# Optimization experiments

Hardware: AMD Instinct MI355X
Metric: run time of the kernel (lower is better)

The kernel has to match this reference:

```python
import jax, jax.numpy as jnp
import numpy as np

D_MODEL = 1024
NUM_HEADS = 16
HEAD_DIM = D_MODEL // NUM_HEADS
FFN_HIDDEN = 4096
EPS = 1e-5


def setup_inputs() -> dict:
    key = jax.random.key(0)
    ks = jax.random.split(key, 7)
    s = 0.02
    return {
        "x": jax.random.normal(ks[0], (2, 2048, D_MODEL), dtype=jnp.float32),
        "W_qkv": jax.random.normal(ks[1], (D_MODEL, 3 * D_MODEL), dtype=jnp.float32) * s,
        "b_qkv": jnp.zeros((3 * D_MODEL,), dtype=jnp.float32),
        "W_o": jax.random.normal(ks[2], (D_MODEL, D_MODEL), dtype=jnp.float32) * s,
        "b_o": jnp.zeros((D_MODEL,), dtype=jnp.float32),
        "gamma1": jnp.ones((D_MODEL,), dtype=jnp.float32),
        "beta1": jnp.zeros((D_MODEL,), dtype=jnp.float32),
        "W1": jax.random.normal(ks[3], (D_MODEL, FFN_HIDDEN), dtype=jnp.float32) * s,
        "b1": jnp.zeros((FFN_HIDDEN,), dtype=jnp.float32),
        "W2": jax.random.normal(ks[4], (FFN_HIDDEN, D_MODEL), dtype=jnp.float32) * s,
        "b2": jnp.zeros((D_MODEL,), dtype=jnp.float32),
        "gamma2": jnp.ones((D_MODEL,), dtype=jnp.float32),
        "beta2": jnp.zeros((D_MODEL,), dtype=jnp.float32),
    }


def _layernorm(x, gamma, beta):
    mean = jnp.mean(x, axis=-1, keepdims=True)
    var = jnp.mean((x - mean) ** 2, axis=-1, keepdims=True)
    return gamma * (x - mean) / jnp.sqrt(var + EPS) + beta


def reference(x, W_qkv, b_qkv, W_o, b_o, gamma1, beta1, W1, b1, W2, b2, gamma2, beta2):
    B, S, D = x.shape
    # ---- multi-head attention ----
    qkv = x @ W_qkv + b_qkv                       # [B,S,3D]
    qkv = qkv.reshape(B, S, NUM_HEADS, 3 * HEAD_DIM).transpose(0, 2, 1, 3)  # [B,H,S,3hd]
    q, k, v = jnp.split(qkv, 3, axis=-1)          # each [B,H,S,hd]
    scores = jnp.einsum("bhqd,bhkd->bhqk", q, k) / np.sqrt(HEAD_DIM)
    attn = jax.nn.softmax(scores, axis=-1)
    vals = jnp.einsum("bhqk,bhkd->bhqd", attn, v)
    vals = vals.transpose(0, 2, 1, 3).reshape(B, S, D)
    attn_out = vals @ W_o + b_o
    # dropout disabled (eval mode)
    h = _layernorm(attn_out + x, gamma1, beta1)
    # ---- position-wise FFN (dropout before relu per source, disabled) ----
    ffn = jax.nn.relu(h @ W1 + b1) @ W2 + b2
    return _layernorm(ffn + h, gamma2, beta2)
```

## Files before the change

### kernel.cpp

```cpp
#include <hip/hip_runtime.h>
#include <stdint.h>

typedef float v4f __attribute__((ext_vector_type(4)));
typedef __bf16 v8bf __attribute__((ext_vector_type(8)));
typedef __bf16 v4bf __attribute__((ext_vector_type(4)));
typedef unsigned short v8us __attribute__((ext_vector_type(8)));
typedef unsigned short v4us __attribute__((ext_vector_type(4)));

__device__ __forceinline__ float b2f(unsigned short u) {
    union { float f; uint32_t i; } x; x.i = ((uint32_t)u) << 16; return x.f;
}
__device__ __forceinline__ unsigned short f2b(float f) {
    union { float f; uint32_t u; } x; x.f = f;
    uint32_t r = x.u + 0x7fffu + ((x.u >> 16) & 1u);
    return (unsigned short)(r >> 16);
}

__device__ __forceinline__ void gload16(const unsigned short* g, unsigned short* l) {
    __builtin_amdgcn_global_load_lds(
        (const __attribute__((address_space(1))) void*)g,
        (__attribute__((address_space(3))) void*)l,
        16, 0, 0);
}

__device__ __forceinline__ void transpose_tile(
    const float* __restrict__ W, unsigned short* __restrict__ WT,
    int K, int N, int kb, int nb, int tid)
{
    __shared__ unsigned short t[64][65];
    const int r = tid >> 4, c4 = (tid & 15) * 4;
    #pragma unroll
    for (int i = 0; i < 4; ++i) {
        int k = r + i * 16;
        float4 v = *(const float4*)&W[(size_t)(kb + k) * N + nb + c4];
        t[c4 + 0][k] = f2b(v.x);
        t[c4 + 1][k] = f2b(v.y);
        t[c4 + 2][k] = f2b(v.z);
        t[c4 + 3][k] = f2b(v.w);
    }
    __syncthreads();
    #pragma unroll
    for (int i = 0; i < 4; ++i) {
        int n = r + i * 16;
        v4us o = {t[n][c4], t[n][c4 + 1], t[n][c4 + 2], t[n][c4 + 3]};
        *(v4us*)&WT[(size_t)(nb + n) * K + kb + c4] = o;
    }
}

__global__ __launch_bounds__(256) void prep_fused(
    const float* __restrict__ x, unsigned short* __restrict__ xb,
    const float* __restrict__ Wqkv, unsigned short* __restrict__ WqkvT,
    const float* __restrict__ W1, unsigned short* __restrict__ W1T,
    const float* __restrict__ Wo, unsigned short* __restrict__ WoT)
{
    const int b = blockIdx.x, tid = threadIdx.x;
    if (b < 4096) {
        int i = (b * 256 + tid) * 4;
        float4 v = *(const float4*)&x[i];
        v4us o = {f2b(v.x), f2b(v.y), f2b(v.z), f2b(v.w)};
        *(v4us*)&xb[i] = o;
    } else if (b < 4096 + 768) {
        int lb = b - 4096;
        transpose_tile(Wqkv, WqkvT, 1024, 3072, (lb / 48) * 64, (lb % 48) * 64, tid);
    } else if (b < 4096 + 768 + 1024) {
        int lb = b - 4096 - 768;
        transpose_tile(W1, W1T, 1024, 4096, (lb / 64) * 64, (lb % 64) * 64, tid);
    } else {
        int lb = b - 4096 - 768 - 1024;
        transpose_tile(Wo, WoT, 1024, 1024, (lb / 16) * 64, (lb % 16) * 64, tid);
    }
}

__global__ __launch_bounds__(256) void transpose_to_bt(
    const float* __restrict__ W, unsigned short* __restrict__ WT, int K, int N)
{
    transpose_tile(W, WT, K, N, blockIdx.y * 64, blockIdx.x * 64, threadIdx.x);
}

__device__ __forceinline__ void xcd_swizzle(int& bm, int& bn) {
    int NB = gridDim.x, MB = gridDim.y;
    int flat = blockIdx.x + NB * blockIdx.y;
    int xcd = flat & 7, j = flat >> 3;
    int MBand = MB >> 3;
    bm = xcd * MBand + (j % MBand);
    bn = j / MBand;
}

__global__ __launch_bounds__(256) void gemm_bt_n64(
    const unsigned short* __restrict__ A, const unsigned short* __restrict__ BT,
    const float* __restrict__ bias, unsigned short* __restrict__ C,
    int M, int N, int K, int relu)
{
    __shared__ __align__(16) unsigned short sA0[2][128 * 32];
    __shared__ __align__(16) unsigned short sB0[2][64 * 32];
    __shared__ __align__(16) unsigned short sA1[2][128 * 32];
    __shared__ __align__(16) unsigned short sB1[2][64 * 32];
    const int tid  = threadIdx.x;
    const int wave = tid >> 6, lane = tid & 63;
    const int wm = wave >> 1, wn = wave & 1;
    const int quad = lane >> 4, l16 = lane & 15;
    int bm, bn;
    xcd_swizzle(bm, bn);

    const int srow = lane >> 2, scol = (lane & 3) * 8;
    const unsigned short* ga0 = A  + (size_t)(bm * 128 + (wave * 2 + 0) * 16 + srow) * K + scol;
    const unsigned short* ga1 = A  + (size_t)(bm * 128 + (wave * 2 + 1) * 16 + srow) * K + scol;
    const unsigned short* gb0 = BT + (size_t)(bn * 64 + wave * 16 + srow) * K + scol;
    const int oa0 = (wave * 2 + 0) * 512 + lane * 8;
    const int oa1 = (wave * 2 + 1) * 512 + lane * 8;
    const int ob  = wave * 512 + lane * 8;

    v8us aR0[2][2], bR0[2], aR1[2][2], bR1[2];
    #pragma unroll
    for (int c = 0; c < 2; ++c) {
        aR0[c][0] = *(const v8us*)(ga0 + c * 32);
        aR0[c][1] = *(const v8us*)(ga1 + c * 32);
        bR0[c]    = *(const v8us*)(gb0 + c * 32);
        aR1[c][0] = *(const v8us*)(ga0 + 64 + c * 32);
        aR1[c][1] = *(const v8us*)(ga1 + 64 + c * 32);
        bR1[c]    = *(const v8us*)(gb0 + 64 + c * 32);
    }

    v4f acc[4][2];
    #pragma unroll
    for (int i = 0; i < 4; ++i)
        #pragma unroll
        for (int j = 0; j < 2; ++j)
            acc[i][j] = (v4f){0.f, 0.f, 0.f, 0.f};

    for (int kt = 0; kt < K; kt += 128) {
        #pragma unroll
        for (int c = 0; c < 2; ++c) {
            *(v8us*)&sA0[c][oa0] = aR0[c][0];
            *(v8us*)&sA0[c][oa1] = aR0[c][1];
            *(v8us*)&sB0[c][ob]  = bR0[c];
        }
        __syncthreads();
        if (kt + 128 < K) {
            const int kn = kt + 128;
            #pragma unroll
            for (int c = 0; c < 2; ++c) {
                aR0[c][0] = *(const v8us*)(ga0 + kn + c * 32);
                aR0[c][1] = *(const v8us*)(ga1 + kn + c * 32);
                bR0[c]    = *(const v8us*)(gb0 + kn + c * 32);
            }
        }
        #pragma unroll
        for (int c = 0; c < 2; ++c) {
            v8bf af[4], bfr[2];
            #pragma unroll
            for (int mt = 0; mt < 4; ++mt)
                af[mt] = *(const v8bf*)&sA0[c][(wm * 64 + mt * 16 + l16) * 32 + quad * 8];
            #pragma unroll
            for (int nt = 0; nt < 2; ++nt)
                bfr[nt] = *(const v8bf*)&sB0[c][(wn * 32 + nt * 16 + l16) * 32 + quad * 8];
            #pragma unroll
            for (int mt = 0; mt < 4; ++mt)
                #pragma unroll
                for (int nt = 0; nt < 2; ++nt)
                    acc[mt][nt] = __builtin_amdgcn_mfma_f32_16x16x32_bf16(
                        af[mt], bfr[nt], acc[mt][nt], 0, 0, 0);
        }

        #pragma unroll
        for (int c = 0; c < 2; ++c) {
            *(v8us*)&sA1[c][oa0] = aR1[c][0];
            *(v8us*)&sA1[c][oa1] = aR1[c][1];
            *(v8us*)&sB1[c][ob]  = bR1[c];
        }
        __syncthreads();
        if (kt + 192 < K) {
            const int kn = kt + 192;
            #pragma unroll
            for (int c = 0; c < 2; ++c) {
                aR1[c][0] = *(const v8us*)(ga0 + kn + c * 32);
                aR1[c][1] = *(const v8us*)(ga1 + kn + c * 32);
                bR1[c]    = *(const v8us*)(gb0 + kn + c * 32);
            }
        }
        #pragma unroll
        for (int c = 0; c < 2; ++c) {
            v8bf af[4], bfr[2];
            #pragma unroll
            for (int mt = 0; mt < 4; ++mt)
                af[mt] = *(const v8bf*)&sA1[c][(wm * 64 + mt * 16 + l16) * 32 + quad * 8];
            #pragma unroll
            for (int nt = 0; nt < 2; ++nt)
                bfr[nt] = *(const v8bf*)&sB1[c][(wn * 32 + nt * 16 + l16) * 32 + quad * 8];
            #pragma unroll
            for (int mt = 0; mt < 4; ++mt)
                #pragma unroll
                for (int nt = 0; nt < 2; ++nt)
                    acc[mt][nt] = __builtin_amdgcn_mfma_f32_16x16x32_bf16(
                        af[mt], bfr[nt], acc[mt][nt], 0, 0, 0);
        }
    }

    #pragma unroll
    for (int mt = 0; mt < 4; ++mt) {
        #pragma unroll
        for (int nt = 0; nt < 2; ++nt) {
            int col = bn * 64 + wn * 32 + nt * 16 + l16;
            float bv = bias ? bias[col] : 0.f;
            #pragma unroll
            for (int r = 0; r < 4; ++r) {
                int row = bm * 128 + wm * 64 + mt * 16 + quad * 4 + r;
                float v = acc[mt][nt][r] + bv;
                if (relu) v = fmaxf(v, 0.f);
                C[(size_t)row * N + col] = f2b(v);
            }
        }
    }
}

template<int SPLIT_V>
__global__ __launch_bounds__(512) void gemm256(
    const unsigned short* __restrict__ A, const unsigned short* __restrict__ BT,
    const float* __restrict__ bias, unsigned short* __restrict__ C,
    unsigned short* __restrict__ VT, int M, int N, int K, int relu)
{
    __shared__ __align__(16) unsigned short sA[2][256 * 64];
    __shared__ __align__(16) unsigned short sB[2][256 * 64];
    const int tid  = threadIdx.x;
    const int wave = tid >> 6, lane = tid & 63;
    const int wm = wave >> 2, wn = wave & 3;
    const int quad = lane >> 4, l16 = lane & 15;
    int bm, bn;
    xcd_swizzle(bm, bn);

    const int srow = lane >> 3;
    const int scol = ((lane & 7) * 8) ^ ((lane & 32) ? 16 : 0);
    size_t aoff[4], boff[4];
    #pragma unroll
    for (int j = 0; j < 4; ++j) {
        int r = wave * 32 + j * 8 + srow;
        aoff[j] = (size_t)(bm * 256 + r) * K + scol;
        boff[j] = (size_t)(bn * 256 + r) * K + scol;
    }
    const int lds0 = wave * 32 * 64;

    const int ksw = (quad * 8) ^ ((l16 & 4) ? 16 : 0);

    v4f acc[8][4];
    #pragma unroll
    for (int i = 0; i < 8; ++i)
        #pragma unroll
        for (int j = 0; j < 4; ++j)
            acc[i][j] = (v4f){0.f, 0.f, 0.f, 0.f};

    const int NT = K >> 6;
    #pragma unroll
    for (int j = 0; j < 4; ++j) {
        gload16(A  + aoff[j], &sA[0][lds0 + j * 512]);
        gload16(BT + boff[j], &sB[0][lds0 + j * 512]);
    }
    __syncthreads();

    for (int t = 0; t < NT; ++t) {
        const int buf = t & 1;
        if (t + 1 < NT) {
            const int ktn = (t + 1) << 6;
            #pragma unroll
            for (int j = 0; j < 4; ++j) {
                gload16(A  + aoff[j] + ktn, &sA[buf ^ 1][lds0 + j * 512]);
                gload16(BT + boff[j] + ktn, &sB[buf ^ 1][lds0 + j * 512]);
            }
        }

        v8bf bfr[4][2];
        #pragma unroll
        for (int nt2 = 0; nt2 < 4; ++nt2)
            #pragma unroll
            for (int kc = 0; kc < 2; ++kc)
                bfr[nt2][kc] = *(const v8bf*)&sB[buf][
                    (wn * 64 + nt2 * 16 + l16) * 64 + kc * 32 + ksw];
        #pragma unroll
        for (int mq = 0; mq < 2; ++mq) {
            v8bf af[4][2];
            #pragma unroll
            for (int mt2 = 0; mt2 < 4; ++mt2)
                #pragma unroll
                for (int kc = 0; kc < 2; ++kc)
                    af[mt2][kc] = *(const v8bf*)&sA[buf][
                        (wm * 128 + mq * 64 + mt2 * 16 + l16) * 64 + kc * 32 + ksw];
            #pragma unroll
            for (int mt2 = 0; mt2 < 4; ++mt2)
                #pragma unroll
                for (int nt2 = 0; nt2 < 4; ++nt2)
                    #pragma unroll
                    for (int kc = 0; kc < 2; ++kc)
                        acc[mq * 4 + mt2][nt2] =
                            __builtin_amdgcn_mfma_f32_16x16x32_bf16(
                                af[mt2][kc], bfr[nt2][kc],
                                acc[mq * 4 + mt2][nt2], 0, 0, 0);
        }
        __syncthreads();
    }

    #pragma unroll
    for (int mt = 0; mt < 8; ++mt) {
        int row = bm * 256 + wm * 128 + mt * 16 + quad * 4;
        #pragma unroll
        for (int nt = 0; nt < 4; ++nt) {
            int c0 = bn * 256 + wn * 64 + nt * 16;
            int col = c0 + l16;
            float bv = bias ? bias[col] : 0.f;
            if (SPLIT_V && (c0 % 192) >= 128) {
                int hh = c0 / 192;
                int d  = (c0 % 192) - 128 + l16;
                int bb = row >> 11;
                int s  = row & 2047;
                v4us st;
                #pragma unroll
                for (int r = 0; r < 4; ++r)
                    st[r] = f2b(acc[mt][nt][r] + bv);
                *(v4us*)&VT[((size_t)(bb * 16 + hh) * 64 + d) * 2048 + s] = st;
            } else {
                float qs = (SPLIT_V && (c0 % 192) < 64) ? 0.18033688f : 1.0f;
                #pragma unroll
                for (int r = 0; r < 4; ++r) {
                    float v = (acc[mt][nt][r] + bv) * qs;
                    if (relu) v = fmaxf(v, 0.f);
                    C[(size_t)(row + r) * N + col] = f2b(v);
                }
            }
        }
    }
}

__global__ __launch_bounds__(512) void attn_mfma(
    const unsigned short* __restrict__ qkv, const unsigned short* __restrict__ VT,
    unsigned short* __restrict__ av)
{
    __shared__ __align__(16) unsigned short sK[2][64 * 72];
    __shared__ __align__(16) unsigned short sVT[2][64 * 72];
    __shared__ __align__(16) unsigned short sP[8][16 * 72];
    const int tid  = threadIdx.x;
    const int wave = tid >> 6, lane = tid & 63;
    const int quad = lane >> 4, l16 = lane & 15;
    const int blk = blockIdx.x;
    const int xcd = blk & 7, local = blk >> 3;
    const int bh = xcd * 4 + (local & 3);
    const int qb = local >> 2;
    const int h = bh & 15, b = bh >> 4;
    const int row0 = b * 2048;
    const int qbase = row0 + qb * 128 + wave * 16;
    const size_t qoff = (size_t)h * 192;
    const size_t koff = qoff + 64;

    v8bf qf[2];
    #pragma unroll
    for (int kc = 0; kc < 2; ++kc)
        qf[kc] = *(const v8bf*)&qkv[(size_t)(qbase + l16) * 3072
                                    + qoff + kc * 32 + quad * 8];

    v4f o[4];
    #pragma unroll
    for (int dt = 0; dt < 4; ++dt)
        o[dt] = (v4f){0.f, 0.f, 0.f, 0.f};
    float ll = 0.f;

    const int k_key = tid >> 3, k_oct = (tid & 7) * 8;
    const unsigned short* gK = qkv + (size_t)(row0 + k_key) * 3072 + koff + k_oct;
    const unsigned short* gV = VT + ((size_t)bh * 64 + k_key) * 2048 + k_oct;
    const size_t stepK = (size_t)64 * 3072;
    const size_t stepV = 64;

    v8us kreg = *(const v8us*)gK;
    v8us vreg = *(const v8us*)gV;
    gK += stepK; gV += stepV;

    for (int kt = 0; kt < 32; ++kt) {
        const int cur = kt & 1;
        *(v8us*)&sK[cur][k_key * 72 + k_oct]  = kreg;
        *(v8us*)&sVT[cur][k_key * 72 + k_oct] = vreg;
        __syncthreads();
        if (kt < 31) {
            kreg = *(const v8us*)gK;
            vreg = *(const v8us*)gV;
            gK += stepK; gV += stepV;
        }

        v4f sc[4];
        #pragma unroll
        for (int kk = 0; kk < 4; ++kk) {
            sc[kk] = (v4f){0.f, 0.f, 0.f, 0.f};
            #pragma unroll
            for (int kc = 0; kc < 2; ++kc) {
                v8bf ak = *(const v8bf*)&sK[cur][(kk * 16 + l16) * 72 + kc * 32 + quad * 8];
                sc[kk] = __builtin_amdgcn_mfma_f32_16x16x32_bf16(
                    ak, qf[kc], sc[kk], 0, 0, 0);
            }
        }

        float ps = 0.f;
        #pragma unroll
        for (int kk = 0; kk < 4; ++kk) {
            v4bf pk;
            #pragma unroll
            for (int rr = 0; rr < 4; ++rr) {
                float p = __builtin_amdgcn_exp2f(sc[kk][rr]);
                ps += p;
                pk[rr] = (__bf16)p;
            }
            *(v4bf*)&sP[wave][l16 * 72 + kk * 16 + quad * 4] = pk;
        }
        ll += ps;

        __asm__ volatile("s_waitcnt lgkmcnt(0)" ::: "memory");

        #pragma unroll
        for (int c = 0; c < 2; ++c) {
            union { v8bf v; v8us u; } u;
            u.u = *(const v8us*)&sP[wave][l16 * 72 + c * 32 + quad * 8];
            v8bf pb = u.v;
            #pragma unroll
            for (int dt = 0; dt < 4; ++dt) {
                v8bf va = *(const v8bf*)&sVT[cur][(dt * 16 + l16) * 72 + c * 32 + quad * 8];
                o[dt] = __builtin_amdgcn_mfma_f32_16x16x32_bf16(
                    va, pb, o[dt], 0, 0, 0);
            }
        }
    }

    float l = ll;
    l += __shfl_xor(l, 16, 64);
    l += __shfl_xor(l, 32, 64);
    float inv = 1.f / l;
    int qrow = qbase + l16;
    #pragma unroll
    for (int dt = 0; dt < 4; ++dt) {
        v4bf st;
        #pragma unroll
        for (int rr = 0; rr < 4; ++rr)
            st[rr] = (__bf16)(o[dt][rr] * inv);
        *(v4bf*)&av[(size_t)qrow * 1024 + h * 64 + dt * 16 + quad * 4] = st;
    }
}

template<int RES_F32, int OUT_F32>
__global__ __launch_bounds__(256) void ln_fused(
    const unsigned short* __restrict__ a, const void* __restrict__ residv,
    const float* __restrict__ gamma, const float* __restrict__ beta,
    void* __restrict__ outv)
{
    const int row = blockIdx.x, tid = threadIdx.x;
    const size_t base = (size_t)row * 1024;
    const int c0 = tid * 4;
    ushort4 avv = *(const ushort4*)&a[base + c0];
    float y[4];
    if (RES_F32) {
        float4 rv = *(const float4*)((const float*)residv + base + c0);
        y[0] = b2f(avv.x) + rv.x;
        y[1] = b2f(avv.y) + rv.y;
        y[2] = b2f(avv.z) + rv.z;
        y[3] = b2f(avv.w) + rv.w;
    } else {
        ushort4 rv = *(const ushort4*)((const unsigned short*)residv + base + c0);
        y[0] = b2f(avv.x) + b2f(rv.x);
        y[1] = b2f(avv.y) + b2f(rv.y);
        y[2] = b2f(avv.z) + b2f(rv.z);
        y[3] = b2f(avv.w) + b2f(rv.w);
    }
    float s  = y[0] + y[1] + y[2] + y[3];
    float ss = y[0]*y[0] + y[1]*y[1] + y[2]*y[2] + y[3]*y[3];
    #pragma unroll
    for (int off = 32; off; off >>= 1) {
        s  += __shfl_xor(s, off, 64);
        ss += __shfl_xor(ss, off, 64);
    }
    __shared__ float red[8];
    int wave = tid >> 6, lane = tid & 63;
    if (lane == 0) { red[wave] = s; red[4 + wave] = ss; }
    __syncthreads();
    s  = red[0] + red[1] + red[2] + red[3];
    ss = red[4] + red[5] + red[6] + red[7];
    float mean = s * (1.f / 1024.f);
    float var  = ss * (1.f / 1024.f) - mean * mean;
    float rstd = rsqrtf(var + 1e-5f);
    float4 gv = *(const float4*)&gamma[c0];
    float4 bv = *(const float4*)&beta[c0];
    float r0 = gv.x * (y[0] - mean) * rstd + bv.x;
    float r1 = gv.y * (y[1] - mean) * rstd + bv.y;
    float r2 = gv.z * (y[2] - mean) * rstd + bv.z;
    float r3 = gv.w * (y[3] - mean) * rstd + bv.w;
    if (OUT_F32) {
        float4 ov = {r0, r1, r2, r3};
        *(float4*)((float*)outv + base + c0) = ov;
    } else {
        ushort4 ov;
        ov.x = f2b(r0); ov.y = f2b(r1); ov.z = f2b(r2); ov.w = f2b(r3);
        *(ushort4*)((unsigned short*)outv + base + c0) = ov;
    }
}

extern "C" void kernel_launch(void* const* d_in, const int* in_sizes, int n_in,
                              void* d_out, int out_size, void* d_ws, size_t ws_size,
                              hipStream_t stream)
{
    (void)in_sizes; (void)n_in; (void)out_size; (void)ws_size;
    const float* x    = (const float*)d_in[0];
    const float* Wqkv = (const float*)d_in[1];
    const float* bqkv = (const float*)d_in[2];
    const float* Wo   = (const float*)d_in[3];
    const float* bo   = (const float*)d_in[4];
    const float* g1   = (const float*)d_in[5];
    const float* be1  = (const float*)d_in[6];
    const float* W1   = (const float*)d_in[7];
    const float* b1   = (const float*)d_in[8];
    const float* W2   = (const float*)d_in[9];
    const float* b2   = (const float*)d_in[10];
    const float* g2   = (const float*)d_in[11];
    const float* be2  = (const float*)d_in[12];
    float* out = (float*)d_out;

    unsigned short* R0 = (unsigned short*)d_ws;
    unsigned short* R1 = R0 + (size_t)16 * 1024 * 1024;
    unsigned short* R2 = R1 + (size_t)4 * 1024 * 1024;
    unsigned short* R3 = R2 + (size_t)4 * 1024 * 1024;
    unsigned short* WqkvT = R0 + (size_t)12 * 1024 * 1024;
    unsigned short* WoT   = R0 + (size_t)15 * 1024 * 1024;

    const int M = 4096;
    dim3 blk(256);

    prep_fused<<<dim3(4096 + 768 + 1024 + 256), blk, 0, stream>>>(
        x, R2, Wqkv, WqkvT, W1, R3, Wo, WoT);
    gemm256<1><<<dim3(12, 16), dim3(512), 0, stream>>>(R2, WqkvT, bqkv, R0, R1, M, 3072, 1024, 0);
    attn_mfma<<<dim3(512), dim3(512), 0, stream>>>(R0, R1, R2);
    gemm_bt_n64<<<dim3(16, 32), blk, 0, stream>>>(R2, WoT, bo, R1, M, 1024, 1024, 0);
    ln_fused<1, 0><<<dim3(4096), blk, 0, stream>>>(R1, x, g1, be1, R1);
    transpose_to_bt<<<dim3(16, 64), blk, 0, stream>>>(W2, R2, 4096, 1024);
    gemm256<0><<<dim3(16, 16), dim3(512), 0, stream>>>(R1, R3, b1, R0, nullptr, M, 4096, 1024, 1);
    gemm_bt_n64<<<dim3(16, 32), blk, 0, stream>>>(R0, R2, b2, R3, M, 1024, 4096, 0);
    ln_fused<0, 1><<<dim3(4096), blk, 0, stream>>>(R3, R1, g2, be2, out);
}
```

Baseline: 337.2 us.

## Switch gemm256 to triple-buffered K=32 tiles with explicit waitcnt pipelining

Changes the 256x256 GEMM mainloop from double-buffered 64-wide K tiles to triple-buffered 32-wide K tiles. Global-to-LDS loads are issued two stages ahead and gated with explicit vmcnt waits and raw barriers instead of __syncthreads. MFMA issue priority is raised with s_setprio. The XOR swizzle on LDS reads is dropped, which risks more bank conflicts, and the smaller K step doubles the number of barriers per K.

New measurement: 360.2 us. 1.07x slower.

```diff
diff --git a/kernel.cpp b/kernel.cpp
--- a/kernel.cpp
+++ b/kernel.cpp
@@ -219,8 +219,8 @@
     const float* __restrict__ bias, unsigned short* __restrict__ C,
     unsigned short* __restrict__ VT, int M, int N, int K, int relu)
 {
-    __shared__ __align__(16) unsigned short sA[2][256 * 64];
-    __shared__ __align__(16) unsigned short sB[2][256 * 64];
+    __shared__ __align__(16) unsigned short sA[3][256 * 32];
+    __shared__ __align__(16) unsigned short sB[3][256 * 32];
     const int tid  = threadIdx.x;
     const int wave = tid >> 6, lane = tid & 63;
     const int wm = wave >> 2, wn = wave & 3;
@@ -228,18 +228,15 @@
     int bm, bn;
     xcd_swizzle(bm, bn);
 
-    const int srow = lane >> 3;
-    const int scol = ((lane & 7) * 8) ^ ((lane & 32) ? 16 : 0);
-    size_t aoff[4], boff[4];
-    #pragma unroll
-    for (int j = 0; j < 4; ++j) {
-        int r = wave * 32 + j * 8 + srow;
+    const int srow = lane >> 2, scol = (lane & 3) * 8;
+    size_t aoff[2], boff[2];
+    #pragma unroll
+    for (int j = 0; j < 2; ++j) {
+        int r = wave * 32 + j * 16 + srow;
         aoff[j] = (size_t)(bm * 256 + r) * K + scol;
         boff[j] = (size_t)(bn * 256 + r) * K + scol;
     }
-    const int lds0 = wave * 32 * 64;
-
-    const int ksw = (quad * 8) ^ ((l16 & 4) ? 16 : 0);
+    const int lds0 = wave * 32 * 32;
 
     v4f acc[8][4];
     #pragma unroll
@@ -248,53 +245,60 @@
         for (int j = 0; j < 4; ++j)
             acc[i][j] = (v4f){0.f, 0.f, 0.f, 0.f};
 
-    const int NT = K >> 6;
-    #pragma unroll
-    for (int j = 0; j < 4; ++j) {
-        gload16(A  + aoff[j], &sA[0][lds0 + j * 512]);
-        gload16(BT + boff[j], &sB[0][lds0 + j * 512]);
-    }
-    __syncthreads();
-
+    const int NT = K >> 5;
+
+    #pragma unroll
+    for (int j = 0; j < 2; ++j) {
+        gload16(A  + aoff[j],      &sA[0][lds0 + j * 512]);
+        gload16(BT + boff[j],      &sB[0][lds0 + j * 512]);
+    }
+    #pragma unroll
+    for (int j = 0; j < 2; ++j) {
+        gload16(A  + aoff[j] + 32, &sA[1][lds0 + j * 512]);
+        gload16(BT + boff[j] + 32, &sB[1][lds0 + j * 512]);
+    }
+
+    int buf = 0;
     for (int t = 0; t < NT; ++t) {
-        const int buf = t & 1;
-        if (t + 1 < NT) {
-            const int ktn = (t + 1) << 6;
-            #pragma unroll
-            for (int j = 0; j < 4; ++j) {
-                gload16(A  + aoff[j] + ktn, &sA[buf ^ 1][lds0 + j * 512]);
-                gload16(BT + boff[j] + ktn, &sB[buf ^ 1][lds0 + j * 512]);
-            }
-        }
-
-        v8bf bfr[4][2];
+        if (t + 2 < NT) {
+            const int b2 = (buf + 2 >= 3) ? buf - 1 : buf + 2;
+            const size_t ko = (size_t)(t + 2) * 32;
+            #pragma unroll
+            for (int j = 0; j < 2; ++j) {
+                gload16(A  + aoff[j] + ko, &sA[b2][lds0 + j * 512]);
+                gload16(BT + boff[j] + ko, &sB[b2][lds0 + j * 512]);
+            }
+        }
+        if (t + 2 < NT)      asm volatile("s_waitcnt vmcnt(8)" ::: "memory");
+        else if (t + 1 < NT) asm volatile("s_waitcnt vmcnt(4)" ::: "memory");
+        else                 asm volatile("s_waitcnt vmcnt(0)" ::: "memory");
+        __builtin_amdgcn_s_barrier();
+
+        const unsigned short* pA = &sA[buf][0];
+        const unsigned short* pB = &sB[buf][0];
+        v8bf bfr[4];
         #pragma unroll
         for (int nt2 = 0; nt2 < 4; ++nt2)
-            #pragma unroll
-            for (int kc = 0; kc < 2; ++kc)
-                bfr[nt2][kc] = *(const v8bf*)&sB[buf][
-                    (wn * 64 + nt2 * 16 + l16) * 64 + kc * 32 + ksw];
-        #pragma unroll
-        for (int mq = 0; mq < 2; ++mq) {
-            v8bf af[4][2];
-            #pragma unroll
-            for (int mt2 = 0; mt2 < 4; ++mt2)
-                #pragma unroll
-                for (int kc = 0; kc < 2; ++kc)
-                    af[mt2][kc] = *(const v8bf*)&sA[buf][
-                        (wm * 128 + mq * 64 + mt2 * 16 + l16) * 64 + kc * 32 + ksw];
-            #pragma unroll
-            for (int mt2 = 0; mt2 < 4; ++mt2)
-                #pragma unroll
-                for (int nt2 = 0; nt2 < 4; ++nt2)
-                    #pragma unroll
-                    for (int kc = 0; kc < 2; ++kc)
-                        acc[mq * 4 + mt2][nt2] =
-                            __builtin_amdgcn_mfma_f32_16x16x32_bf16(
-                                af[mt2][kc], bfr[nt2][kc],
-                                acc[mq * 4 + mt2][nt2], 0, 0, 0);
-        }
-        __syncthreads();
+            bfr[nt2] = *(const v8bf*)&pB[(wn * 64 + nt2 * 16 + l16) * 32 + quad * 8];
+        v8bf af[8];
+        #pragma unroll
+        for (int mt2 = 0; mt2 < 8; ++mt2)
+            af[mt2] = *(const v8bf*)&pA[(wm * 128 + mt2 * 16 + l16) * 32 + quad * 8];
+
+        __builtin_amdgcn_s_setprio(1);
+        #pragma unroll
+        for (int mt2 = 0; mt2 < 8; ++mt2)
+            #pragma unroll
+            for (int nt2 = 0; nt2 < 4; ++nt2)
+                acc[mt2][nt2] = __builtin_amdgcn_mfma_f32_16x16x32_bf16(
+                    af[mt2], bfr[nt2], acc[mt2][nt2], 0, 0, 0);
+        __builtin_amdgcn_s_setprio(0);
+
+        asm volatile("s_waitcnt lgkmcnt(0)" ::: "memory");
+        __builtin_amdgcn_sched_barrier(0);
+        __builtin_amdgcn_s_barrier();
+
+        buf = (buf == 2) ? 0 : buf + 1;
     }
 
     #pragma unroll
```
